# Optimization experiments

Hardware: AMD Instinct MI355X
Metric: run time of the kernel (lower is better)

## Reference

```python
import jax, jax.numpy as jnp
import numpy as np


def setup_inputs() -> dict:
    key = jax.random.key(0)
    k1, k2, *kw = jax.random.split(key, 12)
    N, E = 10000, 320000
    D_IN, D_HID, D_EMB, D_PRED = 2, 128, 256, 128

    def lin(k, fan_in, fan_out):
        bound = 1.0 / np.sqrt(fan_in)
        kw_, kb_ = jax.random.split(k)
        W = jax.random.uniform(kw_, (fan_in, fan_out), jnp.float32, -bound, bound)
        b = jax.random.uniform(kb_, (fan_out,), jnp.float32, -bound, bound)
        return W, b

    W1, b1 = lin(kw[0], D_IN, D_HID)
    W2, b2 = lin(kw[1], D_HID, D_EMB)
    Wp1, bp1 = lin(kw[2], D_EMB, D_PRED)
    Wp2, bp2 = lin(kw[3], D_PRED, 1)

    src = jax.random.randint(k1, (E,), 0, N, dtype=jnp.int32)
    dst = jax.random.randint(k2, (E,), 0, N, dtype=jnp.int32)
    return {
        "W1": W1, "b1": b1, "W2": W2, "b2": b2,
        "Wp1": Wp1, "bp1": bp1, "Wp2": Wp2, "bp2": bp2,
        "src": src, "dst": dst, "num_nodes": N,
    }


def reference(W1, b1, W2, b2, Wp1, bp1, Wp2, bp2, src, dst, num_nodes):
    N = num_nodes
    E = src.shape[0]
    ones = jnp.ones((E,), jnp.float32)
    # node features = [in_degree, out_degree]  -> [N, 2]
    in_deg = jax.ops.segment_sum(ones, dst, num_segments=N)
    out_deg = jax.ops.segment_sum(ones, src, num_segments=N)
    x = jnp.stack([in_deg, out_deg], axis=1)

    def gcn_agg(h):
        # sum of messages from source nodes into destination nodes (SpMM-like)
        return jax.ops.segment_sum(h[src], dst, num_segments=N)

    h = jax.nn.relu(gcn_agg(x) @ W1 + b1)        # [N, 128]
    h = gcn_agg(h) @ W2 + b2                     # [N, 256]
    h = jax.nn.relu(h)
    graph_embedding = jnp.sum(h, axis=0)         # [256] (dgl.sum_nodes, single graph)
    m = jax.nn.relu(graph_embedding @ Wp1 + bp1)
    metric = m @ Wp2 + bp2                       # [1]
    return (graph_embedding, metric)
```

## Files before the change

kernel.cpp:

```cpp
#include <hip/hip_runtime.h>

#define N_NODES 10000
#define CAPLOG 7
#define CAP 128
#define NPART 16
#define NBH 128
#define TBH 512
#define TSTRIDE 132

__global__ __launch_bounds__(TBH) void hist_kernel(const int* __restrict__ src,
                                                   const int* __restrict__ dst,
                                                   unsigned int* __restrict__ cnt,
                                                   float* __restrict__ ge_p,
                                                   unsigned int* __restrict__ done,
                                                   int E) {
  __shared__ unsigned int hist[N_NODES];
  const int tid = threadIdx.x, bid = blockIdx.x;
  for (int i = tid; i < N_NODES; i += TBH) hist[i] = 0;
  if (bid < NPART && tid < 256) ge_p[(bid << 8) + tid] = 0.f;
  if (bid == NPART && tid == 0) *done = 0u;
  __syncthreads();
  const int chunk = (E + NBH - 1) / NBH;
  const int e0 = bid * chunk, e1 = min(E, e0 + chunk);
  for (int e = e0 + tid; e < e1; e += TBH) {
    atomicAdd(&hist[dst[e]], 1u);
    atomicAdd(&hist[src[e]], 0x10000u);
  }
  __syncthreads();
  unsigned int* outb = cnt + (size_t)bid * N_NODES;
  for (int i = tid; i < N_NODES; i += TBH) outb[i] = hist[i];
}

__global__ __launch_bounds__(256) void scan_kernel(const unsigned int* __restrict__ cnt,
                                                   unsigned int* __restrict__ off,
                                                   unsigned int* __restrict__ pack) {
  const int n = blockIdx.x * 256 + threadIdx.x;
  if (n >= N_NODES) return;
  unsigned run = 0;
#pragma unroll 8
  for (int b = 0; b < NBH; ++b) {
    unsigned v = cnt[(size_t)b * N_NODES + n];
    off[(size_t)b * N_NODES + n] = run;
    run += v;
  }
  pack[n] = run;
}

__global__ __launch_bounds__(TBH) void scatter_kernel(const int* __restrict__ src,
                                                      const int* __restrict__ dst,
                                                      const unsigned int* __restrict__ off,
                                                      unsigned short* __restrict__ slots,
                                                      int E) {
  __shared__ unsigned int cur[N_NODES];
  const int tid = threadIdx.x, bid = blockIdx.x;
  const unsigned int* ob = off + (size_t)bid * N_NODES;
  for (int i = tid; i < N_NODES; i += TBH) cur[i] = ob[i];
  __syncthreads();
  const int chunk = (E + NBH - 1) / NBH;
  const int e0 = bid * chunk, e1 = min(E, e0 + chunk);
  for (int e = e0 + tid; e < e1; e += TBH) {
    int d = dst[e];
    unsigned idx = atomicAdd(&cur[d], 1u) & 0xFFFFu;
    if (idx < CAP) slots[(d << CAPLOG) + idx] = (unsigned short)src[e];
  }
}

__global__ __launch_bounds__(256) void agg1_kernel(const unsigned int* __restrict__ pack,
                                                   const unsigned short* __restrict__ slots,
                                                   unsigned int* __restrict__ a) {
  const int tid = threadIdx.x;
  const int hw = tid >> 5, hl = tid & 31;
  const int node = blockIdx.x * 8 + hw;
  const int deg = min((int)(pack[node] & 0xFFFFu), CAP);
  const int base = node << CAPLOG;
  unsigned acc = 0u;
  for (int e = hl; e < deg; e += 32) acc += pack[slots[base + e]];
#pragma unroll
  for (int off = 16; off > 0; off >>= 1) acc += (unsigned)__shfl_xor((int)acc, off, 32);
  if (hl == 0) a[node] = acc;
}

#define FMA_ROW(aR0, aR1, aR2, aR3, t)                                       \
  aR0 = fmaf(t.x, w0.x, aR0); aR0 = fmaf(t.y, w1.x, aR0);                    \
  aR0 = fmaf(t.z, w2v.x, aR0); aR0 = fmaf(t.w, w3.x, aR0);                   \
  aR1 = fmaf(t.x, w0.y, aR1); aR1 = fmaf(t.y, w1.y, aR1);                    \
  aR1 = fmaf(t.z, w2v.y, aR1); aR1 = fmaf(t.w, w3.y, aR1);                   \
  aR2 = fmaf(t.x, w0.z, aR2); aR2 = fmaf(t.y, w1.z, aR2);                    \
  aR2 = fmaf(t.z, w2v.z, aR2); aR2 = fmaf(t.w, w3.z, aR2);                   \
  aR3 = fmaf(t.x, w0.w, aR3); aR3 = fmaf(t.y, w1.w, aR3);                    \
  aR3 = fmaf(t.z, w2v.w, aR3); aR3 = fmaf(t.w, w3.w, aR3);

__global__ __launch_bounds__(256, 4) void agg2gemm2_kernel(const unsigned int* __restrict__ pack,
                                                           const unsigned short* __restrict__ slots,
                                                           const unsigned int* __restrict__ a,
                                                           const float* __restrict__ W1,
                                                           const float* __restrict__ b1,
                                                           const float* __restrict__ W2,
                                                           const float* __restrict__ b2,
                                                           const float* __restrict__ Wp1,
                                                           const float* __restrict__ bp1,
                                                           const float* __restrict__ Wp2,
                                                           const float* __restrict__ bp2,
                                                           float* __restrict__ ge_p,
                                                           unsigned int* __restrict__ done,
                                                           float* __restrict__ out) {
  __shared__ float2 s_a[16][CAP + 1];
  __shared__ float s_t[16 * TSTRIDE];
  __shared__ float s_red[4][256];
  __shared__ float s_ge[256];
  __shared__ float s_m[256];
  __shared__ int s_last;
  const int tid = threadIdx.x, bid = blockIdx.x;
  const int hw = tid >> 5, hl = tid & 31;

#pragma unroll
  for (int nn = 0; nn < 2; ++nn) {
    const int row = hw * 2 + nn;
    const int node = bid * 16 + row;
    const int deg = min((int)(pack[node] & 0xFFFFu), CAP);
    const int base = node << CAPLOG;
    for (int e = hl; e < deg; e += 32) {
      const unsigned v = a[slots[base + e]];
      s_a[row][e] = make_float2((float)(v & 0xFFFFu), (float)(v >> 16));
    }
  }

  float w10[4], w11[4], bb[4];
#pragma unroll
  for (int c = 0; c < 4; ++c) {
    w10[c] = W1[4 * hl + c];
    w11[c] = W1[128 + 4 * hl + c];
    bb[c] = b1[4 * hl + c];
  }
  __syncthreads();

#pragma unroll
  for (int nn = 0; nn < 2; ++nn) {
    const int row = hw * 2 + nn;
    const int node = bid * 16 + row;
    const int deg = min((int)(pack[node] & 0xFFFFu), CAP);
    float acc0 = 0.f, acc1 = 0.f, acc2 = 0.f, acc3 = 0.f;
#pragma unroll 4
    for (int j = 0; j < deg; ++j) {
      const float2 av = s_a[row][j];
      acc0 += fmaxf(fmaf(av.x, w10[0], fmaf(av.y, w11[0], bb[0])), 0.f);
      acc1 += fmaxf(fmaf(av.x, w10[1], fmaf(av.y, w11[1], bb[1])), 0.f);
      acc2 += fmaxf(fmaf(av.x, w10[2], fmaf(av.y, w11[2], bb[2])), 0.f);
      acc3 += fmaxf(fmaf(av.x, w10[3], fmaf(av.y, w11[3], bb[3])), 0.f);
    }
    float* tr = s_t + row * TSTRIDE + 4 * hl;
    tr[0] = acc0; tr[1] = acc1; tr[2] = acc2; tr[3] = acc3;
  }
  __syncthreads();

  const int jq = tid & 63, ng = tid >> 6;
  const int j = jq << 2;
  const float* tb = s_t + (ng << 2) * TSTRIDE;
  float a00 = 0.f, a01 = 0.f, a02 = 0.f, a03 = 0.f;
  float a10 = 0.f, a11 = 0.f, a12 = 0.f, a13 = 0.f;
  float a20 = 0.f, a21 = 0.f, a22 = 0.f, a23 = 0.f;
  float a30 = 0.f, a31 = 0.f, a32 = 0.f, a33 = 0.f;
#pragma unroll 4
  for (int k = 0; k < 128; k += 4) {
    const float4 w0 = *(const float4*)(W2 + (k + 0) * 256 + j);
    const float4 w1 = *(const float4*)(W2 + (k + 1) * 256 + j);
    const float4 w2v = *(const float4*)(W2 + (k + 2) * 256 + j);
    const float4 w3 = *(const float4*)(W2 + (k + 3) * 256 + j);
    const float4 t0 = *(const float4*)(tb + 0 * TSTRIDE + k);
    const float4 t1 = *(const float4*)(tb + 1 * TSTRIDE + k);
    const float4 t2 = *(const float4*)(tb + 2 * TSTRIDE + k);
    const float4 t3 = *(const float4*)(tb + 3 * TSTRIDE + k);
    FMA_ROW(a00, a01, a02, a03, t0)
    FMA_ROW(a10, a11, a12, a13, t1)
    FMA_ROW(a20, a21, a22, a23, t2)
    FMA_ROW(a30, a31, a32, a33, t3)
  }

  const float4 bj = *(const float4*)(b2 + j);
  float4 part;
  part.x = fmaxf(a00 + bj.x, 0.f) + fmaxf(a10 + bj.x, 0.f) +
           fmaxf(a20 + bj.x, 0.f) + fmaxf(a30 + bj.x, 0.f);
  part.y = fmaxf(a01 + bj.y, 0.f) + fmaxf(a11 + bj.y, 0.f) +
           fmaxf(a21 + bj.y, 0.f) + fmaxf(a31 + bj.y, 0.f);
  part.z = fmaxf(a02 + bj.z, 0.f) + fmaxf(a12 + bj.z, 0.f) +
           fmaxf(a22 + bj.z, 0.f) + fmaxf(a32 + bj.z, 0.f);
  part.w = fmaxf(a03 + bj.w, 0.f) + fmaxf(a13 + bj.w, 0.f) +
           fmaxf(a23 + bj.w, 0.f) + fmaxf(a33 + bj.w, 0.f);
  *(float4*)(&s_red[ng][j]) = part;
  __syncthreads();
  const float g = (s_red[0][tid] + s_red[1][tid]) + (s_red[2][tid] + s_red[3][tid]);
  atomicAdd(&ge_p[((bid & (NPART - 1)) << 8) + tid], g);

  __syncthreads();
  if (tid == 0) {
    __threadfence();
    s_last = (atomicAdd(done, 1u) == (unsigned)(gridDim.x - 1)) ? 1 : 0;
  }
  __syncthreads();
  if (!s_last) return;

  float gg = 0.f;
#pragma unroll
  for (int p = 0; p < NPART; ++p)
    gg += __hip_atomic_load(&ge_p[p * 256 + tid], __ATOMIC_RELAXED, __HIP_MEMORY_SCOPE_AGENT);
  s_ge[tid] = gg;
  out[tid] = gg;
  __syncthreads();
  const int jh = tid & 127, halfk = tid >> 7;
  float dd = halfk ? 0.f : bp1[jh];
  const int k0 = halfk << 7;
#pragma unroll 8
  for (int k = k0; k < k0 + 128; ++k) dd = fmaf(s_ge[k], Wp1[k * 128 + jh], dd);
  s_m[tid] = dd;
  __syncthreads();
  if (tid < 128) s_m[tid] = fmaxf(s_m[tid] + s_m[tid + 128], 0.f) * Wp2[tid];
  __syncthreads();
  if (tid < 64) {
    float v = s_m[tid] + s_m[tid + 64];
#pragma unroll
    for (int off = 32; off > 0; off >>= 1) v += __shfl_xor(v, off);
    if (tid == 0) out[256] = v + bp2[0];
  }
}

extern "C" void kernel_launch(void* const* d_in, const int* in_sizes, int n_in,
                              void* d_out, int out_size, void* d_ws, size_t ws_size,
                              hipStream_t stream) {
  const float* W1 = (const float*)d_in[0];
  const float* b1 = (const float*)d_in[1];
  const float* W2 = (const float*)d_in[2];
  const float* b2 = (const float*)d_in[3];
  const float* Wp1 = (const float*)d_in[4];
  const float* bp1 = (const float*)d_in[5];
  const float* Wp2 = (const float*)d_in[6];
  const float* bp2 = (const float*)d_in[7];
  const int* src = (const int*)d_in[8];
  const int* dst = (const int*)d_in[9];
  const int E = in_sizes[8];
  const int N = N_NODES;

  char* p = (char*)d_ws;
  float* ge_p = (float*)p;               p += (size_t)NPART * 256 * 4;
  unsigned int* done = (unsigned int*)p; p += 16;
  unsigned int* pack = (unsigned int*)p; p += (size_t)N * 4;
  unsigned int* a = (unsigned int*)p;    p += (size_t)N * 4;
  unsigned short* slots = (unsigned short*)p; p += (size_t)N * CAP * 2;
  unsigned int* cnt = (unsigned int*)p;  p += (size_t)NBH * N * 4;
  unsigned int* off = (unsigned int*)p;
  float* out = (float*)d_out;

  hist_kernel<<<NBH, TBH, 0, stream>>>(src, dst, cnt, ge_p, done, E);
  scan_kernel<<<(N + 255) / 256, 256, 0, stream>>>(cnt, off, pack);
  scatter_kernel<<<NBH, TBH, 0, stream>>>(src, dst, off, slots, E);
  agg1_kernel<<<N / 8, 256, 0, stream>>>(pack, slots, a);
  agg2gemm2_kernel<<<N / 16, 256, 0, stream>>>(pack, slots, a, W1, b1, W2, b2,
                                               Wp1, bp1, Wp2, bp2, ge_p, done, out);
}
```

Before: 139.0 us.

## Split prediction head into a parallel kernel and prefetch W2 rows in GEMM loop

The serial last-block tail of the aggregation/GEMM kernel is removed. A separate 128-block head kernel computes one Wp1 output per block, combining partial sums with wave shuffles and an atomic accumulator plus a done counter, so the head's work is spread across blocks instead of one. The W2 loop in the GEMM is software-pipelined by loading the next four W2 rows while the current ones are used. This also drops the grid-wide done atomic from the big kernel. In exchange it adds one more kernel launch and extra registers for the prefetched weights.

```diff
diff --git a/kernel.cpp b/kernel.cpp
--- a/kernel.cpp
+++ b/kernel.cpp
@@ -7,18 +7,21 @@
 #define NBH 128
 #define TBH 512
 #define TSTRIDE 132
+#define HB 128
 
 __global__ __launch_bounds__(TBH) void hist_kernel(const int* __restrict__ src,
                                                    const int* __restrict__ dst,
                                                    unsigned int* __restrict__ cnt,
                                                    float* __restrict__ ge_p,
+                                                   float* __restrict__ m,
                                                    unsigned int* __restrict__ done,
                                                    int E) {
   __shared__ unsigned int hist[N_NODES];
   const int tid = threadIdx.x, bid = blockIdx.x;
   for (int i = tid; i < N_NODES; i += TBH) hist[i] = 0;
   if (bid < NPART && tid < 256) ge_p[(bid << 8) + tid] = 0.f;
-  if (bid == NPART && tid == 0) *done = 0u;
+  if (bid == NPART && tid < HB) m[tid] = 0.f;
+  if (bid == NPART && tid == HB) *done = 0u;
   __syncthreads();
   const int chunk = (E + NBH - 1) / NBH;
   const int e0 = bid * chunk, e1 = min(E, e0 + chunk);
@@ -97,19 +100,10 @@
                                                            const float* __restrict__ b1,
                                                            const float* __restrict__ W2,
                                                            const float* __restrict__ b2,
-                                                           const float* __restrict__ Wp1,
-                                                           const float* __restrict__ bp1,
-                                                           const float* __restrict__ Wp2,
-                                                           const float* __restrict__ bp2,
-                                                           float* __restrict__ ge_p,
-                                                           unsigned int* __restrict__ done,
-                                                           float* __restrict__ out) {
+                                                           float* __restrict__ ge_p) {
   __shared__ float2 s_a[16][CAP + 1];
   __shared__ float s_t[16 * TSTRIDE];
   __shared__ float s_red[4][256];
-  __shared__ float s_ge[256];
-  __shared__ float s_m[256];
-  __shared__ int s_last;
   const int tid = threadIdx.x, bid = blockIdx.x;
   const int hw = tid >> 5, hl = tid & 31;
 
@@ -156,20 +150,39 @@
   const int jq = tid & 63, ng = tid >> 6;
   const int j = jq << 2;
   const float* tb = s_t + (ng << 2) * TSTRIDE;
+  float4 wc0 = *(const float4*)(W2 + 0 * 256 + j);
+  float4 wc1 = *(const float4*)(W2 + 1 * 256 + j);
+  float4 wc2 = *(const float4*)(W2 + 2 * 256 + j);
+  float4 wc3 = *(const float4*)(W2 + 3 * 256 + j);
   float a00 = 0.f, a01 = 0.f, a02 = 0.f, a03 = 0.f;
   float a10 = 0.f, a11 = 0.f, a12 = 0.f, a13 = 0.f;
   float a20 = 0.f, a21 = 0.f, a22 = 0.f, a23 = 0.f;
   float a30 = 0.f, a31 = 0.f, a32 = 0.f, a33 = 0.f;
 #pragma unroll 4
-  for (int k = 0; k < 128; k += 4) {
-    const float4 w0 = *(const float4*)(W2 + (k + 0) * 256 + j);
-    const float4 w1 = *(const float4*)(W2 + (k + 1) * 256 + j);
-    const float4 w2v = *(const float4*)(W2 + (k + 2) * 256 + j);
-    const float4 w3 = *(const float4*)(W2 + (k + 3) * 256 + j);
+  for (int k = 0; k < 124; k += 4) {
+    const float4 wn0 = *(const float4*)(W2 + (k + 4) * 256 + j);
+    const float4 wn1 = *(const float4*)(W2 + (k + 5) * 256 + j);
+    const float4 wn2 = *(const float4*)(W2 + (k + 6) * 256 + j);
+    const float4 wn3 = *(const float4*)(W2 + (k + 7) * 256 + j);
     const float4 t0 = *(const float4*)(tb + 0 * TSTRIDE + k);
     const float4 t1 = *(const float4*)(tb + 1 * TSTRIDE + k);
     const float4 t2 = *(const float4*)(tb + 2 * TSTRIDE + k);
     const float4 t3 = *(const float4*)(tb + 3 * TSTRIDE + k);
+    {
+      const float4 w0 = wc0, w1 = wc1, w2v = wc2, w3 = wc3;
+      FMA_ROW(a00, a01, a02, a03, t0)
+      FMA_ROW(a10, a11, a12, a13, t1)
+      FMA_ROW(a20, a21, a22, a23, t2)
+      FMA_ROW(a30, a31, a32, a33, t3)
+    }
+    wc0 = wn0; wc1 = wn1; wc2 = wn2; wc3 = wn3;
+  }
+  {
+    const float4 t0 = *(const float4*)(tb + 0 * TSTRIDE + 124);
+    const float4 t1 = *(const float4*)(tb + 1 * TSTRIDE + 124);
+    const float4 t2 = *(const float4*)(tb + 2 * TSTRIDE + 124);
+    const float4 t3 = *(const float4*)(tb + 3 * TSTRIDE + 124);
+    const float4 w0 = wc0, w1 = wc1, w2v = wc2, w3 = wc3;
     FMA_ROW(a00, a01, a02, a03, t0)
     FMA_ROW(a10, a11, a12, a13, t1)
     FMA_ROW(a20, a21, a22, a23, t2)
@@ -190,37 +203,45 @@
   __syncthreads();
   const float g = (s_red[0][tid] + s_red[1][tid]) + (s_red[2][tid] + s_red[3][tid]);
   atomicAdd(&ge_p[((bid & (NPART - 1)) << 8) + tid], g);
-
+}
+
+__global__ __launch_bounds__(256) void head_kernel(const float* __restrict__ ge_p,
+                                                   const float* __restrict__ Wp1,
+                                                   const float* __restrict__ bp1,
+                                                   const float* __restrict__ Wp2,
+                                                   const float* __restrict__ bp2,
+                                                   float* __restrict__ m,
+                                                   unsigned int* __restrict__ done,
+                                                   float* __restrict__ out) {
+  __shared__ float s_r[4];
+  __shared__ int s_last;
+  const int tid = threadIdx.x, j = blockIdx.x;
+  float g = 0.f;
+#pragma unroll
+  for (int p = 0; p < NPART; ++p) g += ge_p[p * 256 + tid];
+  if (j == 0) out[tid] = g;
+  float part = g * Wp1[tid * 128 + j];
+#pragma unroll
+  for (int o = 32; o > 0; o >>= 1) part += __shfl_xor(part, o);
+  if ((tid & 63) == 0) s_r[tid >> 6] = part;
   __syncthreads();
   if (tid == 0) {
+    const float mj = bp1[j] + (s_r[0] + s_r[1]) + (s_r[2] + s_r[3]);
+    atomicAdd(&m[j], mj);
     __threadfence();
-    s_last = (atomicAdd(done, 1u) == (unsigned)(gridDim.x - 1)) ? 1 : 0;
+    s_last = (atomicAdd(done, 1u) == HB - 1) ? 1 : 0;
   }
   __syncthreads();
   if (!s_last) return;
-
-  float gg = 0.f;
-#pragma unroll
-  for (int p = 0; p < NPART; ++p)
-    gg += __hip_atomic_load(&ge_p[p * 256 + tid], __ATOMIC_RELAXED, __HIP_MEMORY_SCOPE_AGENT);
-  s_ge[tid] = gg;
-  out[tid] = gg;
-  __syncthreads();
-  const int jh = tid & 127, halfk = tid >> 7;
-  float dd = halfk ? 0.f : bp1[jh];
-  const int k0 = halfk << 7;
-#pragma unroll 8
-  for (int k = k0; k < k0 + 128; ++k) dd = fmaf(s_ge[k], Wp1[k * 128 + jh], dd);
-  s_m[tid] = dd;
-  __syncthreads();
-  if (tid < 128) s_m[tid] = fmaxf(s_m[tid] + s_m[tid + 128], 0.f) * Wp2[tid];
-  __syncthreads();
-  if (tid < 64) {
-    float v = s_m[tid] + s_m[tid + 64];
-#pragma unroll
-    for (int off = 32; off > 0; off >>= 1) v += __shfl_xor(v, off);
-    if (tid == 0) out[256] = v + bp2[0];
-  }
+  float v = 0.f;
+  if (tid < 128)
+    v = fmaxf(__hip_atomic_load(&m[tid], __ATOMIC_RELAXED, __HIP_MEMORY_SCOPE_AGENT), 0.f) *
+        Wp2[tid];
+#pragma unroll
+  for (int o = 32; o > 0; o >>= 1) v += __shfl_xor(v, o);
+  if ((tid & 63) == 0) s_r[tid >> 6] = v;
+  __syncthreads();
+  if (tid == 0) out[256] = s_r[0] + s_r[1] + bp2[0];
 }
 
 extern "C" void kernel_launch(void* const* d_in, const int* in_sizes, int n_in,
@@ -241,6 +262,7 @@
 
   char* p = (char*)d_ws;
   float* ge_p = (float*)p;               p += (size_t)NPART * 256 * 4;
+  float* m = (float*)p;                  p += HB * 4;
   unsigned int* done = (unsigned int*)p; p += 16;
   unsigned int* pack = (unsigned int*)p; p += (size_t)N * 4;
   unsigned int* a = (unsigned int*)p;    p += (size_t)N * 4;
@@ -249,10 +271,10 @@
   unsigned int* off = (unsigned int*)p;
   float* out = (float*)d_out;
 
-  hist_kernel<<<NBH, TBH, 0, stream>>>(src, dst, cnt, ge_p, done, E);
+  hist_kernel<<<NBH, TBH, 0, stream>>>(src, dst, cnt, ge_p, m, done, E);
   scan_kernel<<<(N + 255) / 256, 256, 0, stream>>>(cnt, off, pack);
   scatter_kernel<<<NBH, TBH, 0, stream>>>(src, dst, off, slots, E);
   agg1_kernel<<<N / 8, 256, 0, stream>>>(pack, slots, a);
-  agg2gemm2_kernel<<<N / 16, 256, 0, stream>>>(pack, slots, a, W1, b1, W2, b2,
-                                               Wp1, bp1, Wp2, bp2, ge_p, done, out);
-}
+  agg2gemm2_kernel<<<N / 16, 256, 0, stream>>>(pack, slots, a, W1, b1, W2, b2, ge_p);
+  head_kernel<<<HB, 256, 0, stream>>>(ge_p, Wp1, bp1, Wp2, bp2, m, done, out);
+}
```

Measured after the change: 129.4 us. -6.9%, faster.
